# Optimization experiments

Measured on AMD Instinct MI355X. Metric: run time of the kernel, lower is better.

## Reference

```python
import jax, jax.numpy as jnp
import numpy as np

N, T, DIN, DH = 100000, 512, 256, 256


def setup_inputs() -> dict:
    key = jax.random.key(0)
    ks = jax.random.split(key, 7)
    s_in = 1.0 / np.sqrt(DH)  # torch GRU init scale
    X = jax.random.normal(ks[0], (N, DIN), dtype=jnp.float32)
    H = (jax.random.uniform(ks[1], (N, T)) < 0.02).astype(jnp.float32)
    W_ih = jax.random.uniform(ks[2], (3 * DH, DIN), minval=-s_in, maxval=s_in, dtype=jnp.float32)
    W_hh = jax.random.uniform(ks[3], (3 * DH, DH), minval=-s_in, maxval=s_in, dtype=jnp.float32)
    b_ih = jax.random.uniform(ks[4], (3 * DH,), minval=-s_in, maxval=s_in, dtype=jnp.float32)
    b_hh = jax.random.uniform(ks[5], (3 * DH,), minval=-s_in, maxval=s_in, dtype=jnp.float32)
    w_att = jax.random.uniform(ks[6], (DH,), minval=-s_in, maxval=s_in, dtype=jnp.float32)
    return {"X": X, "H": H, "W_ih": W_ih, "W_hh": W_hh, "b_ih": b_ih, "b_hh": b_hh, "w_att": w_att}


def _gru(visit_emb, W_ih, W_hh, b_ih, b_hh):
    # torch GRU gate order: r, z, n
    dh = W_hh.shape[1]
    gx = visit_emb @ W_ih.T + b_ih  # [T, 3H] precomputed input projections

    def step(h, gx_t):
        gh = h @ W_hh.T + b_hh  # [3H]
        r = jax.nn.sigmoid(gx_t[:dh] + gh[:dh])
        z = jax.nn.sigmoid(gx_t[dh:2 * dh] + gh[dh:2 * dh])
        n = jnp.tanh(gx_t[2 * dh:] + r * gh[2 * dh:])
        h_new = (1.0 - z) * n + z * h
        return h_new, h_new

    h0 = jnp.zeros((dh,), dtype=visit_emb.dtype)
    _, hs = jax.lax.scan(step, h0, gx)
    return hs  # [T, H]


def reference(X, H, W_ih, W_hh, b_ih, b_hh, w_att):
    visit_emb = H.T @ X  # [T, Din] incidence aggregation
    hidden = _gru(visit_emb, W_ih, W_hh, b_ih, b_hh)  # [T, H]
    alpha = jax.nn.softmax(hidden @ w_att, axis=0)  # [T]
    # diag(alpha) @ hidden summed over T == alpha-weighted sum
    return jnp.einsum("t,th->h", alpha, hidden)
```

## Files before the change

### kernel.cpp

```cpp
#include <hip/hip_runtime.h>
#include <hip/hip_bf16.h>

#define N_ROWS 100000
#define T_DIM  512
#define DIN    256
#define DH     256
#define KC     800
#define NSTEP  25
#define NCHUNK 125

typedef __attribute__((ext_vector_type(8))) short s16x8;
typedef __attribute__((ext_vector_type(4))) float f32x4;

static __device__ __forceinline__ unsigned bf16pair(float lo, float hi) {
  unsigned a = __builtin_bit_cast(unsigned, lo);
  unsigned b = __builtin_bit_cast(unsigned, hi);
  a = (a + 0x7fffu + ((a >> 16) & 1u)) >> 16;
  b = (b + 0x7fffu + ((b >> 16) & 1u)) & 0xffff0000u;
  return a | b;
}

__global__ __launch_bounds__(512, 2) void k_agg_mfma(
    const float* __restrict__ X, const float* __restrict__ Hm,
    float* __restrict__ ve, float* __restrict__ ve_part, int use_part)
{
  __shared__ unsigned smem[8192];
  const int tid  = threadIdx.x;
  const int mt   = blockIdx.x & 1;
  const int kc   = blockIdx.x >> 1;
  const int m0   = mt * 256;
  const int k0   = kc * KC;
  const int lane = tid & 63;
  const int wv   = tid >> 6;
  const int wm   = wv >> 2, wn = wv & 3;

  f32x4 acc[8][4] = {};

  const int kp0 = tid >> 6;
  const int kp1 = kp0 + 8;
  const int gg  = tid & 63;

  float4 ra0, ra1, ra2, ra3, rb0, rb1, rb2, rb3;

  auto load_tile = [&](int kt) {
    const size_t kb = (size_t)(k0 + kt * 32);
    const float* pa0 = &Hm[(kb + 2 * kp0) * T_DIM + m0 + gg * 4];
    ra0 = *(const float4*)pa0;
    ra1 = *(const float4*)(pa0 + T_DIM);
    const float* pa1 = &Hm[(kb + 2 * kp1) * T_DIM + m0 + gg * 4];
    ra2 = *(const float4*)pa1;
    ra3 = *(const float4*)(pa1 + T_DIM);
    const float* pb0 = &X[(kb + 2 * kp0) * DIN + gg * 4];
    rb0 = *(const float4*)pb0;
    rb1 = *(const float4*)(pb0 + DIN);
    const float* pb1 = &X[(kb + 2 * kp1) * DIN + gg * 4];
    rb2 = *(const float4*)pb1;
    rb3 = *(const float4*)(pb1 + DIN);
  };

  auto store_tile = [&]() {
#pragma unroll
    for (int d = 0; d < 4; ++d) {
      const int m  = gg * 4 + d;
      const int sw = d << 2;
      smem[m * 16 + (kp0 ^ sw)]        = bf16pair(((const float*)&ra0)[d], ((const float*)&ra1)[d]);
      smem[m * 16 + (kp1 ^ sw)]        = bf16pair(((const float*)&ra2)[d], ((const float*)&ra3)[d]);
      smem[4096 + m * 16 + (kp0 ^ sw)] = bf16pair(((const float*)&rb0)[d], ((const float*)&rb1)[d]);
      smem[4096 + m * 16 + (kp1 ^ sw)] = bf16pair(((const float*)&rb2)[d], ((const float*)&rb3)[d]);
    }
  };

  auto compute = [&]() {
    const uint4* sv = (const uint4*)smem;
    s16x8 af[8], bfr[4];
#pragma unroll
    for (int fm = 0; fm < 8; ++fm) {
      const int m = wm * 128 + fm * 16 + (lane & 15);
      af[fm] = __builtin_bit_cast(s16x8, sv[m * 4 + ((lane >> 4) ^ (m & 3))]);
    }
#pragma unroll
    for (int fn = 0; fn < 4; ++fn) {
      const int n = wn * 64 + fn * 16 + (lane & 15);
      bfr[fn] = __builtin_bit_cast(s16x8, sv[1024 + n * 4 + ((lane >> 4) ^ (n & 3))]);
    }
#pragma unroll
    for (int fm = 0; fm < 8; ++fm)
#pragma unroll
      for (int fn = 0; fn < 4; ++fn)
        acc[fm][fn] = __builtin_amdgcn_mfma_f32_16x16x32_bf16(af[fm], bfr[fn], acc[fm][fn], 0, 0, 0);
  };

  load_tile(0);
  store_tile();
  for (int kt = 0; kt < NSTEP; ++kt) {
    __syncthreads();
    if (kt + 1 < NSTEP) load_tile(kt + 1);
    compute();
    __syncthreads();
    if (kt + 1 < NSTEP) store_tile();
  }

  if (use_part) {
    float* dst = ve_part + (size_t)kc * (512 * 256);
#pragma unroll
    for (int fm = 0; fm < 8; ++fm) {
      const int r0 = m0 + wm * 128 + fm * 16 + (lane >> 4) * 4;
#pragma unroll
      for (int fn = 0; fn < 4; ++fn) {
        const int cc = wn * 64 + fn * 16 + (lane & 15);
#pragma unroll
        for (int q = 0; q < 4; ++q)
          dst[(size_t)(r0 + q) * 256 + cc] = acc[fm][fn][q];
      }
    }
  } else {
#pragma unroll
    for (int fm = 0; fm < 8; ++fm) {
      const int r0 = m0 + wm * 128 + fm * 16 + (lane >> 4) * 4;
#pragma unroll
      for (int fn = 0; fn < 4; ++fn) {
        const int cc = wn * 64 + fn * 16 + (lane & 15);
#pragma unroll
        for (int q = 0; q < 4; ++q)
          atomicAdd(&ve[(size_t)(r0 + q) * 256 + cc], acc[fm][fn][q]);
      }
    }
  }
}

__global__ __launch_bounds__(256) void k_gx(
    const float* __restrict__ vesrc, int npart,
    const float* __restrict__ Wih, const float* __restrict__ bih,
    float* __restrict__ gx)
{
  __shared__ float vl[DIN];
  const int t = blockIdx.x, j = threadIdx.x;
  float s = 0.f;
  for (int p = 0; p < npart; ++p) s += vesrc[(size_t)p * (512 * 256) + t * DIN + j];
  vl[j] = s;
  __syncthreads();
  float a0 = bih[j], a1 = bih[256 + j], a2 = bih[512 + j];
  const float* __restrict__ w0 = &Wih[(size_t)j * DIN];
  const float* __restrict__ w1 = &Wih[(size_t)(j + 256) * DIN];
  const float* __restrict__ w2 = &Wih[(size_t)(j + 512) * DIN];
#pragma unroll 4
  for (int k = 0; k < DIN; ++k) {
    const float v = vl[k];
    a0 = fmaf(w0[k], v, a0);
    a1 = fmaf(w1[k], v, a1);
    a2 = fmaf(w2[k], v, a2);
  }
  gx[t * 768 + j]       = a0;
  gx[t * 768 + 256 + j] = a1;
  gx[t * 768 + 512 + j] = a2;
}

__global__ __launch_bounds__(512, 2) void k_gru_att(
    const float* __restrict__ Whh, const float* __restrict__ bhh,
    const float* __restrict__ gx, const float* __restrict__ watt,
    float* __restrict__ hs, float* __restrict__ out)
{
  __shared__ __hip_bfloat16 hb[DH];
  __shared__ float ghs[768];
  __shared__ float bsh[768];
  __shared__ float sc[T_DIM];
  __shared__ float red[2];

  const int tid = threadIdx.x;
  const int w   = tid >> 6;
  const int l   = tid & 63;
  const int lr  = l & 15;
  const int lg  = l >> 4;

  int rowbase[6];
  rowbase[0] = w * 32;       rowbase[1] = w * 32 + 16;
  rowbase[2] = 256 + w * 32; rowbase[3] = 256 + w * 32 + 16;
  rowbase[4] = 512 + w * 32; rowbase[5] = 512 + w * 32 + 16;

  s16x8 wf[6][8];
#pragma unroll
  for (int tt = 0; tt < 6; ++tt) {
    const float* rp = &Whh[(size_t)(rowbase[tt] + lr) * DH + lg * 8];
#pragma unroll
    for (int kb = 0; kb < 8; ++kb) {
      const float4 x0 = *(const float4*)(rp + kb * 32);
      const float4 x1 = *(const float4*)(rp + kb * 32 + 4);
      uint4 uu;
      uu.x = bf16pair(x0.x, x0.y);
      uu.y = bf16pair(x0.z, x0.w);
      uu.z = bf16pair(x1.x, x1.y);
      uu.w = bf16pair(x1.z, x1.w);
      wf[tt][kb] = __builtin_bit_cast(s16x8, uu);
    }
  }

  bsh[tid] = bhh[tid < 768 ? tid : 0];
  if (tid < 256) {
    bsh[512 + tid] = bhh[512 + tid];
    hb[tid] = __float2bfloat16(0.0f);
  }
  float h = 0.f;
  __syncthreads();

  for (int t = 0; t < T_DIM; ++t) {
    float gxr = 0.f, gxz = 0.f, gxn = 0.f;
    if (tid < 256) {
      gxr = gx[t * 768 + tid];
      gxz = gx[t * 768 + 256 + tid];
      gxn = gx[t * 768 + 512 + tid];
    }
    f32x4 acc[6];
#pragma unroll
    for (int tt = 0; tt < 6; ++tt)
      acc[tt] = *(const f32x4*)&bsh[rowbase[tt] + lg * 4];
#pragma unroll
    for (int kb = 0; kb < 8; ++kb) {
      const s16x8 bf = *(const s16x8*)((const char*)hb + kb * 64 + lg * 16);
#pragma unroll
      for (int tt = 0; tt < 6; ++tt)
        acc[tt] = __builtin_amdgcn_mfma_f32_16x16x32_bf16(wf[tt][kb], bf, acc[tt], 0, 0, 0);
    }
    if (lr == 0) {
#pragma unroll
      for (int tt = 0; tt < 6; ++tt)
        *(f32x4*)&ghs[rowbase[tt] + lg * 4] = acc[tt];
    }
    __syncthreads();
    if (tid < 256) {
      const float r = 1.f / (1.f + __expf(-(gxr + ghs[tid])));
      const float z = 1.f / (1.f + __expf(-(gxz + ghs[256 + tid])));
      const float pn = gxn + r * ghs[512 + tid];
      const float n = 2.f / (1.f + __expf(-2.f * pn)) - 1.f;
      h = (1.f - z) * n + z * h;
      hs[t * DH + tid] = h;
      hb[tid] = __float2bfloat16(h);
    }
    __syncthreads();
  }

  {
    const float* __restrict__ hr = &hs[tid * DH];
    float s = 0.f;
#pragma unroll 4
    for (int k = 0; k < DH; k += 4) {
      const float4 hv = *(const float4*)(hr + k);
      const float4 wv4 = *(const float4*)(watt + k);
      s = fmaf(hv.x, wv4.x, s); s = fmaf(hv.y, wv4.y, s);
      s = fmaf(hv.z, wv4.z, s); s = fmaf(hv.w, wv4.w, s);
    }
    sc[tid] = s;
  }
  __syncthreads();
  if (tid < 64) {
    float m = -1e30f;
#pragma unroll
    for (int i = 0; i < 8; ++i) m = fmaxf(m, sc[tid * 8 + i]);
#pragma unroll
    for (int off = 32; off > 0; off >>= 1) m = fmaxf(m, __shfl_down(m, off));
    if (tid == 0) red[0] = m;
  }
  __syncthreads();
  const float M = red[0];
  sc[tid] = __expf(sc[tid] - M);
  __syncthreads();
  if (tid < 64) {
    float s = 0.f;
#pragma unroll
    for (int i = 0; i < 8; ++i) s += sc[tid * 8 + i];
#pragma unroll
    for (int off = 32; off > 0; off >>= 1) s += __shfl_down(s, off);
    if (tid == 0) red[1] = s;
  }
  __syncthreads();
  const float inv = 1.f / red[1];
  {
    const int j = tid & 255, half = tid >> 8;
    float acc = 0.f;
    for (int t = half * 256; t < half * 256 + 256; ++t)
      acc = fmaf(sc[t], hs[t * DH + j], acc);
    bsh[half * 256 + j] = acc;
  }
  __syncthreads();
  if (tid < 256) out[tid] = (bsh[tid] + bsh[256 + tid]) * inv;
}

extern "C" void kernel_launch(void* const* d_in, const int* in_sizes, int n_in,
                              void* d_out, int out_size, void* d_ws, size_t ws_size,
                              hipStream_t stream) {
  const float* X    = (const float*)d_in[0];
  const float* H    = (const float*)d_in[1];
  const float* Wih  = (const float*)d_in[2];
  const float* Whh  = (const float*)d_in[3];
  const float* bih  = (const float*)d_in[4];
  const float* bhh  = (const float*)d_in[5];
  const float* watt = (const float*)d_in[6];
  float* out = (float*)d_out;

  char* ws = (char*)d_ws;
  float* gx      = (float*)ws;
  float* hs      = (float*)(ws + 1572864);
  float* ve      = (float*)(ws + 2097152);
  float* ve_part = (float*)(ws + 2621440);

  const size_t need_part = 2621440 + 65536000;
  const int use_part = (ws_size >= need_part) ? 1 : 0;

  if (!use_part)
    hipMemsetAsync(ve, 0, T_DIM * DIN * sizeof(float), stream);

  k_agg_mfma<<<2 * NCHUNK, 512, 0, stream>>>(X, H, ve, ve_part, use_part);
  k_gx<<<T_DIM, 256, 0, stream>>>(use_part ? ve_part : ve, use_part ? NCHUNK : 1,
                                  Wih, bih, gx);
  k_gru_att<<<1, 512, 0, stream>>>(Whh, bhh, gx, watt, hs, out);
}
```

Baseline: 1.030 ms.

## Split GRU recurrent weights across registers, LDS and streamed global loads

```diff
diff --git a/kernel.cpp b/kernel.cpp
--- a/kernel.cpp
+++ b/kernel.cpp
@@ -155,11 +155,31 @@
   gx[t * 768 + 512 + j] = a2;
 }
 
-__global__ __launch_bounds__(512, 2) void k_gru_att(
-    const float* __restrict__ Whh, const float* __restrict__ bhh,
+__global__ __launch_bounds__(256) void k_pack(
+    const float* __restrict__ Whh, uint4* __restrict__ wpack)
+{
+  const int c = blockIdx.x * 256 + threadIdx.x;
+  const int l = c & 63;
+  const int f = (c >> 6) % 48;
+  const int w = c / (48 * 64);
+  const int s = f >> 3, kb = f & 7;
+  const int row = w * 96 + s * 16 + (l & 15);
+  const int col = kb * 32 + (l >> 4) * 8;
+  const float* p = &Whh[(size_t)row * DH + col];
+  uint4 u;
+  u.x = bf16pair(p[0], p[1]);
+  u.y = bf16pair(p[2], p[3]);
+  u.z = bf16pair(p[4], p[5]);
+  u.w = bf16pair(p[6], p[7]);
+  wpack[c] = u;
+}
+
+__global__ __launch_bounds__(512) void k_gru_att(
+    const uint4* __restrict__ wpack, const float* __restrict__ bhh,
     const float* __restrict__ gx, const float* __restrict__ watt,
     float* __restrict__ hs, float* __restrict__ out)
 {
+  __shared__ uint4 wlds[18 * 8 * 64];
   __shared__ __hip_bfloat16 hb[DH];
   __shared__ float ghs[768];
   __shared__ float bsh[768];
@@ -169,32 +189,25 @@
   const int tid = threadIdx.x;
   const int w   = tid >> 6;
   const int l   = tid & 63;
+  const int lg  = l >> 4;
   const int lr  = l & 15;
-  const int lg  = l >> 4;
-
-  int rowbase[6];
-  rowbase[0] = w * 32;       rowbase[1] = w * 32 + 16;
-  rowbase[2] = 256 + w * 32; rowbase[3] = 256 + w * 32 + 16;
-  rowbase[4] = 512 + w * 32; rowbase[5] = 512 + w * 32 + 16;
-
-  s16x8 wf[6][8];
-#pragma unroll
-  for (int tt = 0; tt < 6; ++tt) {
-    const float* rp = &Whh[(size_t)(rowbase[tt] + lr) * DH + lg * 8];
-#pragma unroll
-    for (int kb = 0; kb < 8; ++kb) {
-      const float4 x0 = *(const float4*)(rp + kb * 32);
-      const float4 x1 = *(const float4*)(rp + kb * 32 + 4);
-      uint4 uu;
-      uu.x = bf16pair(x0.x, x0.y);
-      uu.y = bf16pair(x0.z, x0.w);
-      uu.z = bf16pair(x1.x, x1.y);
-      uu.w = bf16pair(x1.z, x1.w);
-      wf[tt][kb] = __builtin_bit_cast(s16x8, uu);
-    }
-  }
-
-  bsh[tid] = bhh[tid < 768 ? tid : 0];
+
+  const uint4* __restrict__ wsv = wpack + (size_t)w * 48 * 64;
+
+  s16x8 wf[12];
+#pragma unroll
+  for (int s = 0; s < 6; ++s)
+#pragma unroll
+    for (int kb = 0; kb < 2; ++kb)
+      wf[s * 2 + kb] = __builtin_bit_cast(s16x8, wsv[((s << 3) + kb) * 64 + l]);
+
+#pragma unroll
+  for (int j = 0; j < 18; ++j) {
+    const int s = j / 3, kb = 2 + j % 3;
+    wlds[(w * 18 + j) * 64 + l] = wsv[((s << 3) + kb) * 64 + l];
+  }
+
+  bsh[tid] = bhh[tid];
   if (tid < 256) {
     bsh[512 + tid] = bhh[512 + tid];
     hb[tid] = __float2bfloat16(0.0f);
@@ -203,27 +216,55 @@
   __syncthreads();
 
   for (int t = 0; t < T_DIM; ++t) {
+    uint4 st[6];
+#pragma unroll
+    for (int s = 0; s < 6; ++s) st[s] = wsv[((s << 3) + 5) * 64 + l];
+
     float gxr = 0.f, gxz = 0.f, gxn = 0.f;
     if (tid < 256) {
       gxr = gx[t * 768 + tid];
       gxz = gx[t * 768 + 256 + tid];
       gxn = gx[t * 768 + 512 + tid];
     }
+
     f32x4 acc[6];
 #pragma unroll
-    for (int tt = 0; tt < 6; ++tt)
-      acc[tt] = *(const f32x4*)&bsh[rowbase[tt] + lg * 4];
-#pragma unroll
-    for (int kb = 0; kb < 8; ++kb) {
+    for (int s = 0; s < 6; ++s)
+      acc[s] = *(const f32x4*)&bsh[w * 96 + s * 16 + lg * 4];
+
+#pragma unroll
+    for (int kb = 0; kb < 2; ++kb) {
       const s16x8 bf = *(const s16x8*)((const char*)hb + kb * 64 + lg * 16);
 #pragma unroll
-      for (int tt = 0; tt < 6; ++tt)
-        acc[tt] = __builtin_amdgcn_mfma_f32_16x16x32_bf16(wf[tt][kb], bf, acc[tt], 0, 0, 0);
-    }
+      for (int s = 0; s < 6; ++s)
+        acc[s] = __builtin_amdgcn_mfma_f32_16x16x32_bf16(wf[s * 2 + kb], bf, acc[s], 0, 0, 0);
+    }
+#pragma unroll
+    for (int kb = 2; kb < 5; ++kb) {
+      const s16x8 bf = *(const s16x8*)((const char*)hb + kb * 64 + lg * 16);
+#pragma unroll
+      for (int s = 0; s < 6; ++s) {
+        const s16x8 a = __builtin_bit_cast(s16x8, wlds[(w * 18 + s * 3 + (kb - 2)) * 64 + l]);
+        acc[s] = __builtin_amdgcn_mfma_f32_16x16x32_bf16(a, bf, acc[s], 0, 0, 0);
+      }
+    }
+#pragma unroll
+    for (int b = 0; b < 3; ++b) {
+      const int kb = 5 + b;
+      const s16x8 bf = *(const s16x8*)((const char*)hb + kb * 64 + lg * 16);
+#pragma unroll
+      for (int s = 0; s < 6; ++s)
+        acc[s] = __builtin_amdgcn_mfma_f32_16x16x32_bf16(__builtin_bit_cast(s16x8, st[s]), bf, acc[s], 0, 0, 0);
+      if (b < 2) {
+#pragma unroll
+        for (int s = 0; s < 6; ++s) st[s] = wsv[((s << 3) + 6 + b) * 64 + l];
+      }
+    }
+
     if (lr == 0) {
 #pragma unroll
-      for (int tt = 0; tt < 6; ++tt)
-        *(f32x4*)&ghs[rowbase[tt] + lg * 4] = acc[tt];
+      for (int s = 0; s < 6; ++s)
+        *(f32x4*)&ghs[w * 96 + s * 16 + lg * 4] = acc[s];
     }
     __syncthreads();
     if (tid < 256) {
@@ -238,13 +279,15 @@
     __syncthreads();
   }
 
+  if (tid < 256) bsh[tid] = watt[tid];
+  __syncthreads();
   {
-    const float* __restrict__ hr = &hs[tid * DH];
+    const float* __restrict__ hr = &hs[(size_t)tid * DH];
     float s = 0.f;
 #pragma unroll 4
     for (int k = 0; k < DH; k += 4) {
       const float4 hv = *(const float4*)(hr + k);
-      const float4 wv4 = *(const float4*)(watt + k);
+      const float4 wv4 = *(const float4*)(&bsh[k]);
       s = fmaf(hv.x, wv4.x, s); s = fmaf(hv.y, wv4.y, s);
       s = fmaf(hv.z, wv4.z, s); s = fmaf(hv.w, wv4.w, s);
     }
@@ -277,11 +320,11 @@
     const int j = tid & 255, half = tid >> 8;
     float acc = 0.f;
     for (int t = half * 256; t < half * 256 + 256; ++t)
-      acc = fmaf(sc[t], hs[t * DH + j], acc);
-    bsh[half * 256 + j] = acc;
-  }
-  __syncthreads();
-  if (tid < 256) out[tid] = (bsh[tid] + bsh[256 + tid]) * inv;
+      acc = fmaf(sc[t], hs[(size_t)t * DH + j], acc);
+    ghs[half * 256 + j] = acc;
+  }
+  __syncthreads();
+  if (tid < 256) out[tid] = (ghs[tid] + ghs[256 + tid]) * inv;
 }
 
 extern "C" void kernel_launch(void* const* d_in, const int* in_sizes, int n_in,
@@ -300,16 +343,18 @@
   float* gx      = (float*)ws;
   float* hs      = (float*)(ws + 1572864);
   float* ve      = (float*)(ws + 2097152);
-  float* ve_part = (float*)(ws + 2621440);
-
-  const size_t need_part = 2621440 + 65536000;
+  uint4* wpack   = (uint4*)(ws + 2621440);
+  float* ve_part = (float*)(ws + 3014656);
+
+  const size_t need_part = 3014656ull + 65536000ull;
   const int use_part = (ws_size >= need_part) ? 1 : 0;
 
   if (!use_part)
     hipMemsetAsync(ve, 0, T_DIM * DIN * sizeof(float), stream);
 
+  k_pack<<<96, 256, 0, stream>>>(Whh, wpack);
   k_agg_mfma<<<2 * NCHUNK, 512, 0, stream>>>(X, H, ve, ve_part, use_part);
   k_gx<<<T_DIM, 256, 0, stream>>>(use_part ? ve_part : ve, use_part ? NCHUNK : 1,
                                   Wih, bih, gx);
-  k_gru_att<<<1, 512, 0, stream>>>(Whh, bhh, gx, watt, hs, out);
-}
+  k_gru_att<<<1, 512, 0, stream>>>(wpack, bhh, gx, watt, hs, out);
+}
```

Result: no change. 1.027 ms (-0.3%).
